# Performance work log

Measured on AMD Instinct MI355X. Metric: run time of the kernel, lower is better.

## Reference

```python
import jax, jax.numpy as jnp
import numpy as np

UNITS, ORDER, THETA = 1024, 512, 784.0
T, B = 784, 128

def _lmu_AB(order, theta):
    # Legendre delay continuous-time state space, then ZOH discretization (dt=1)
    q = np.arange(order, dtype=np.float64)
    r = (2.0 * q + 1.0)[:, None] / theta
    i, j = np.meshgrid(q, q, indexing='ij')
    A = np.where(i < j, -1.0, (-1.0) ** (i - j + 1.0)) * r
    Bc = ((-1.0) ** q)[:, None] * r
    Ad = np.array(jax.scipy.linalg.expm(jnp.asarray(A, dtype=jnp.float32)), dtype=np.float64)
    Bd = np.linalg.solve(A, (Ad - np.eye(order)) @ Bc)
    # cell stores AT = Ad - I so that m <- m + m@AT^T + u@BT^T == m@Ad^T + u@Bd^T
    return (Ad - np.eye(order)).astype(np.float32), Bd.astype(np.float32)

def setup_inputs() -> dict:
    key = jax.random.key(0)
    ks = jax.random.split(key, 9)
    AT, BT = _lmu_AB(ORDER, THETA)
    xav = np.sqrt(2.0 / (UNITS + ORDER)).astype(np.float32)
    return {
        'inputs': jax.random.normal(ks[0], (T, B, 1), dtype=jnp.float32),
        'e_x': jax.random.normal(ks[1], (1, 1), dtype=jnp.float32),
        'e_h': jax.random.normal(ks[2], (1, UNITS), dtype=jnp.float32) * 0.02,
        'e_m': jax.random.normal(ks[3], (1, ORDER), dtype=jnp.float32) * 0.02,
        'W_x': jax.random.normal(ks[4], (UNITS, 1), dtype=jnp.float32) * 0.1,
        'W_h': jax.random.normal(ks[5], (UNITS, UNITS), dtype=jnp.float32) * 0.02,
        'W_m': jax.random.normal(ks[6], (UNITS, ORDER), dtype=jnp.float32) * xav,
        'AT': jnp.asarray(AT),
        'BT': jnp.asarray(BT),
        'W_dense': jax.random.normal(ks[7], (10, UNITS), dtype=jnp.float32) * 0.03,
        'b_dense': jax.random.normal(ks[8], (10,), dtype=jnp.float32) * 0.01,
    }

def reference(inputs, e_x, e_h, e_m, W_x, W_h, W_m, AT, BT, W_dense, b_dense):
    Bsz = inputs.shape[1]
    h0 = jnp.zeros((Bsz, W_h.shape[0]), inputs.dtype)
    m0 = jnp.zeros((Bsz, AT.shape[0]), inputs.dtype)
    def step(carry, x):  # x: (B, 1)
        h, m = carry
        u = x @ e_x.T + h @ e_h.T + m @ e_m.T            # (B, 1)
        m = m + m @ AT.T + u @ BT.T                       # linear Legendre memory update
        h = jnp.tanh(x @ W_x.T + h @ W_h.T + m @ W_m.T)  # nonlinear hidden update
        return (h, m), None
    (h, m), _ = jax.lax.scan(step, (h0, m0), inputs)
    logits = h @ W_dense.T + b_dense
    return jax.nn.softmax(logits, axis=-1)
```

## Files before the change

kernel.cpp:

```cpp
#include <hip/hip_runtime.h>
#include <hip/hip_fp16.h>
#include <cmath>


typedef _Float16 half8 __attribute__((ext_vector_type(8)));
typedef float floatx4 __attribute__((ext_vector_type(4)));

#define NSTATE   1536
#define BATCH    128
#define TSTEPS   784
#define KTILES   48
#define ISL_WGS  32
#define SLICE_H8 9216
#define LO_SCALE 2048.0f
#define LO_INV   (1.0f / 2048.0f)
#define NWAVES   8
#define KI_W     6

__device__ __align__(16) _Float16 g_Whi[NSTATE * NSTATE];
__device__ __align__(16) _Float16 g_Wlo[NSTATE * NSTATE];
__device__ float    g_wb[NSTATE];
__device__ float    g_WmA[1024 * 512];
__device__ float    g_WmB[1024];
__device__ __align__(16) _Float16 g_Shi[2 * BATCH * NSTATE];
__device__ __align__(16) _Float16 g_Slo[2 * BATCH * NSTATE];
__device__ unsigned g_bar[1024];

__device__ __forceinline__ unsigned poll_rmw(unsigned* p) {
    unsigned old;
    asm volatile("global_atomic_add %0, %1, %2, off sc0\n\ts_waitcnt vmcnt(0)"
                 : "=&v"(old)
                 : "v"(p), "v"(0u)
                 : "memory");
    return old;
}

__device__ __forceinline__ float fast_tanh(float x) {
    float e = __expf(2.f * x);
    return 1.f - 2.f / (e + 1.f);
}

__global__ void prep_wmb(const float* __restrict__ Wm, const float* __restrict__ BT) {
    int row  = blockIdx.x * 4 + (threadIdx.x >> 6);
    int lane = threadIdx.x & 63;
    float s = 0.f;
    for (int c = lane; c < 512; c += 64) s += Wm[row * 512 + c] * BT[c];
    for (int o = 32; o; o >>= 1) s += __shfl_down(s, o);
    if (lane == 0) g_WmB[row] = s;
}

__global__ void prep_wma(const float* __restrict__ Wm, const float* __restrict__ AT) {
    __shared__ float As[32][33], Bs[32][33];
    int d0 = blockIdx.x * 32, i0 = blockIdx.y * 32;
    int tx = threadIdx.x & 31, ty = threadIdx.x >> 5;
    float acc[4];
#pragma unroll
    for (int r = 0; r < 4; ++r) acc[r] = Wm[(i0 + ty + 8 * r) * 512 + d0 + tx];
    for (int c0 = 0; c0 < 512; c0 += 32) {
#pragma unroll
        for (int r = 0; r < 4; ++r) {
            As[ty + 8 * r][tx] = Wm[(i0 + ty + 8 * r) * 512 + c0 + tx];
            Bs[ty + 8 * r][tx] = AT[(c0 + ty + 8 * r) * 512 + d0 + tx];
        }
        __syncthreads();
#pragma unroll
        for (int c = 0; c < 32; ++c)
#pragma unroll
            for (int r = 0; r < 4; ++r) acc[r] += As[ty + 8 * r][c] * Bs[c][tx];
        __syncthreads();
    }
#pragma unroll
    for (int r = 0; r < 4; ++r) g_WmA[(i0 + ty + 8 * r) * 512 + d0 + tx] = acc[r];
}

__global__ void prep_wfull(const float* __restrict__ Wh, const float* __restrict__ AT,
                           const float* __restrict__ BT, const float* __restrict__ eh,
                           const float* __restrict__ em, const float* __restrict__ ex,
                           const float* __restrict__ Wx) {
    int s = blockIdx.x * 256 + threadIdx.x;
    int j8 = s & 7;
    int u = s >> 3;
    int lane = u & 63;
    u >>= 6;
    int nt = u % 3; u /= 3;
    int kt = u % 48;
    int sl = u / 48;
    int n = sl * 48 + nt * 16 + (lane & 15);
    int k = kt * 32 + ((lane >> 4) & 3) * 8 + j8;

    float w;
    if (n < 1024) {
        if (k < 1024) w = Wh[n * 1024 + k] + g_WmB[n] * eh[k];
        else          w = g_WmA[n * 512 + (k - 1024)] + g_WmB[n] * em[k - 1024];
    } else {
        int c = n - 1024;
        if (k < 1024) w = BT[c] * eh[k];
        else {
            int d = k - 1024;
            w = ((c == d) ? 1.f : 0.f) + AT[c * 512 + d] + BT[c] * em[d];
        }
    }
    _Float16 hi = (_Float16)w;
    g_Whi[s] = hi;
    g_Wlo[s] = (_Float16)((w - (float)hi) * LO_SCALE);

    if (s < NSTATE) {
        float b = (s < 1024) ? (Wx[s] + ex[0] * g_WmB[s]) : (BT[s - 1024] * ex[0]);
        g_wb[s] = b;
    }
    if (s < 2 * BATCH * NSTATE) { g_Shi[s] = (_Float16)0.f; g_Slo[s] = (_Float16)0.f; }
    if (s < 1024) g_bar[s] = 0u;
}

__launch_bounds__(512, 2)
__global__ void lmu_persist(const float* __restrict__ inputs) {
    __shared__ half8   lwh[SLICE_H8];
    __shared__ floatx4 red[4 * 3 * 64];
    __shared__ int     s_sl;

    const int tid = threadIdx.x;

    unsigned xcd;
    asm volatile("s_getreg_b32 %0, hwreg(HW_REG_XCC_ID)" : "=s"(xcd));
    xcd &= 7u;
    if (tid == 0) {
        unsigned rank = __hip_atomic_fetch_add(g_bar + 512 + xcd * 64, 1u,
                                               __ATOMIC_RELAXED,
                                               __HIP_MEMORY_SCOPE_WORKGROUP);
        s_sl = (int)(rank & 31u);
    }
    __syncthreads();
    const int isl = (int)xcd;
    const int sl  = s_sl;

    {
        const half8* src = (const half8*)g_Whi + (size_t)sl * SLICE_H8;
        for (int i = tid; i < SLICE_H8; i += 512) lwh[i] = src[i];
    }

    const int lane = tid & 63, wv = tid >> 6;
    const int quad = lane >> 4, l16 = lane & 15;
    const int kt0 = wv * KI_W;
    const int rowA = isl * 16 + l16;
    unsigned* cnt = g_bar + isl * 64;

    const int ncol = sl * 48 + wv * 16 + l16;
    const float wbv = (wv < 3) ? g_wb[ncol] : 0.f;
    const bool do_tanh = (sl * 48 + wv * 16) < 1024;

    half8 wr[KI_W * 3];
    {
        const half8* wlo = (const half8*)g_Wlo + (size_t)sl * SLICE_H8;
#pragma unroll
        for (int ki = 0; ki < KI_W; ++ki)
#pragma unroll
            for (int nt = 0; nt < 3; ++nt)
                wr[ki * 3 + nt] = wlo[((kt0 + ki) * 3 + nt) * 64 + lane];
    }

    __syncthreads();

    int buf = 0;
    for (int t = 0; t < TSTEPS; ++t) {
        const _Float16* shr =
            g_Shi + buf * BATCH * NSTATE + rowA * NSTATE + quad * 8;
        const _Float16* slr =
            g_Slo + buf * BATCH * NSTATE + rowA * NSTATE + quad * 8;

        floatx4 aA[3], aB[3], aC[3];
#pragma unroll
        for (int q = 0; q < 3; ++q) { aA[q] = (floatx4)0.f; aB[q] = (floatx4)0.f; aC[q] = (floatx4)0.f; }

#pragma unroll
        for (int ki = 0; ki < KI_W; ++ki) {
            const int kt = kt0 + ki;
            half8 ah = *(const half8*)(shr + kt * 32);
            half8 al = *(const half8*)(slr + kt * 32);
#pragma unroll
            for (int nt = 0; nt < 3; ++nt) {
                half8 bh = lwh[(kt * 3 + nt) * 64 + lane];
                aA[nt] = __builtin_amdgcn_mfma_f32_16x16x32_f16(ah, bh, aA[nt], 0, 0, 0);
                aB[nt] = __builtin_amdgcn_mfma_f32_16x16x32_f16(al, bh, aB[nt], 0, 0, 0);
                aC[nt] = __builtin_amdgcn_mfma_f32_16x16x32_f16(ah, wr[ki * 3 + nt], aC[nt], 0, 0, 0);
            }
        }

        floatx4 P[3];
#pragma unroll
        for (int nt = 0; nt < 3; ++nt)
            P[nt] = aA[nt] + (aB[nt] + aC[nt]) * LO_INV;
        if (wv < 4) {
#pragma unroll
            for (int nt = 0; nt < 3; ++nt)
                red[((wv & 3) * 3 + nt) * 64 + lane] = P[nt];
        }
        __syncthreads();
        if (wv >= 4) {
#pragma unroll
            for (int nt = 0; nt < 3; ++nt)
                red[((wv & 3) * 3 + nt) * 64 + lane] += P[nt];
        }
        __syncthreads();

        const int nbuf = buf ^ 1;
        if (wv < 3) {
            floatx4 vs = red[(0 * 3 + wv) * 64 + lane] + red[(1 * 3 + wv) * 64 + lane]
                       + red[(2 * 3 + wv) * 64 + lane] + red[(3 * 3 + wv) * 64 + lane];
            _Float16* dh = g_Shi + nbuf * BATCH * NSTATE;
            _Float16* dl = g_Slo + nbuf * BATCH * NSTATE;
            const float* xt = inputs + t * BATCH + isl * 16 + quad * 4;
#pragma unroll
            for (int r = 0; r < 4; ++r) {
                int b = isl * 16 + quad * 4 + r;
                float v = vs[r] + xt[r] * wbv;
                if (do_tanh) v = fast_tanh(v);
                _Float16 hi = (_Float16)v;
                dh[b * NSTATE + ncol] = hi;
                dl[b * NSTATE + ncol] = (_Float16)((v - (float)hi) * LO_SCALE);
            }
        }

        __builtin_amdgcn_fence(__ATOMIC_RELEASE, "workgroup");
        __syncthreads();
        if (tid == 0) {
            __hip_atomic_fetch_add(cnt, 1u, __ATOMIC_RELAXED,
                                   __HIP_MEMORY_SCOPE_WORKGROUP);
            const unsigned target = (unsigned)ISL_WGS * (unsigned)(t + 1);
            int spin = 0;
            while (poll_rmw(cnt) < target) {
                if (++spin > (1 << 18)) break;
            }
        }
        __syncthreads();
        asm volatile("buffer_inv\n\ts_waitcnt vmcnt(0)" ::: "memory");
        __builtin_amdgcn_fence(__ATOMIC_ACQUIRE, "workgroup");
        buf = nbuf;
    }
}

__global__ void lmu_out(const float* __restrict__ Wd, const float* __restrict__ bd,
                        float* __restrict__ out) {
    __shared__ float red[272];
    int b = blockIdx.x;
    const _Float16* sh = g_Shi + b * NSTATE;
    const _Float16* sl = g_Slo + b * NSTATE;
    int tid = threadIdx.x;
    int c = tid & 15, chunk = tid >> 4;
    float part = 0.f;
    if (c < 10) {
        for (int i = chunk * 64; i < chunk * 64 + 64; ++i)
            part += ((float)sh[i] + (float)sl[i] * LO_INV) * Wd[c * 1024 + i];
    }
    red[chunk * 16 + c] = part;
    __syncthreads();
    if (tid < 10) {
        float lg = bd[tid];
        for (int q = 0; q < 16; ++q) lg += red[q * 16 + tid];
        red[256 + tid] = lg;
    }
    __syncthreads();
    if (tid < 10) {
        float mx = red[256];
        for (int q = 1; q < 10; ++q) mx = fmaxf(mx, red[256 + q]);
        float sm = 0.f;
        for (int q = 0; q < 10; ++q) sm += expf(red[256 + q] - mx);
        out[b * 10 + tid] = expf(red[256 + tid] - mx) / sm;
    }
}

extern "C" void kernel_launch(void* const* d_in, const int* in_sizes, int n_in,
                              void* d_out, int out_size, void* d_ws, size_t ws_size,
                              hipStream_t stream) {
    const float* inputs = (const float*)d_in[0];
    const float* e_x    = (const float*)d_in[1];
    const float* e_h    = (const float*)d_in[2];
    const float* e_m    = (const float*)d_in[3];
    const float* W_x    = (const float*)d_in[4];
    const float* W_h    = (const float*)d_in[5];
    const float* W_m    = (const float*)d_in[6];
    const float* AT     = (const float*)d_in[7];
    const float* BT     = (const float*)d_in[8];
    const float* W_d    = (const float*)d_in[9];
    const float* b_d    = (const float*)d_in[10];
    (void)d_ws; (void)ws_size; (void)in_sizes; (void)n_in;

    prep_wmb<<<256, 256, 0, stream>>>(W_m, BT);
    prep_wma<<<dim3(16, 32), 256, 0, stream>>>(W_m, AT);
    prep_wfull<<<9216, 256, 0, stream>>>(W_h, AT, BT, e_h, e_m, e_x, W_x);

    lmu_persist<<<256, 512, 0, stream>>>(inputs);

    lmu_out<<<128, 256, 0, stream>>>(W_d, b_d, (float*)d_out);
}
```

Before: 3.949 ms.

## Split workgroup into two independent pipelines with per-producer flag synchronization

Replaces the per-step all-workgroup counter barrier and __syncthreads with fine-grained flags: each workgroup's half (pipe of 4 waves handling 8 batch rows) waits only on the specific producer slices it reads, and intra-WG reduction uses LDS spin counters instead of block barriers. Each wave now covers 12 k-tiles with half the A rows zeroed, doubling per-wave MFMA work while halving the useful rows. The aim is to cut barrier latency and let the two pipes run decoupled, at the cost of wasted MFMA lanes, more register pressure (36 half8 low-weight registers) and fragile spin-wait ordering.

```diff
diff --git a/kernel.cpp b/kernel.cpp
--- a/kernel.cpp
+++ b/kernel.cpp
@@ -14,8 +14,7 @@
 #define SLICE_H8 9216
 #define LO_SCALE 2048.0f
 #define LO_INV   (1.0f / 2048.0f)
-#define NWAVES   8
-#define KI_W     6
+#define PIPES    2
 
 __device__ __align__(16) _Float16 g_Whi[NSTATE * NSTATE];
 __device__ __align__(16) _Float16 g_Wlo[NSTATE * NSTATE];
@@ -25,6 +24,7 @@
 __device__ __align__(16) _Float16 g_Shi[2 * BATCH * NSTATE];
 __device__ __align__(16) _Float16 g_Slo[2 * BATCH * NSTATE];
 __device__ unsigned g_bar[1024];
+__device__ unsigned g_flags[PIPES * 8 * 32 * 64];
 
 __device__ __forceinline__ unsigned poll_rmw(unsigned* p) {
     unsigned old;
@@ -33,6 +33,19 @@
                  : "v"(p), "v"(0u)
                  : "memory");
     return old;
+}
+
+__device__ __forceinline__ void lds_arrive(unsigned* c) {
+    if ((threadIdx.x & 63) == 0)
+        __hip_atomic_fetch_add(c, 1u, __ATOMIC_RELEASE,
+                               __HIP_MEMORY_SCOPE_WORKGROUP);
+}
+__device__ __forceinline__ void lds_wait(unsigned* c, unsigned tgt) {
+    int spin = 0;
+    while (__hip_atomic_load(c, __ATOMIC_ACQUIRE,
+                             __HIP_MEMORY_SCOPE_WORKGROUP) < tgt) {
+        if (++spin > (1 << 20)) break;
+    }
 }
 
 __device__ __forceinline__ float fast_tanh(float x) {
@@ -110,13 +123,15 @@
     }
     if (s < 2 * BATCH * NSTATE) { g_Shi[s] = (_Float16)0.f; g_Slo[s] = (_Float16)0.f; }
     if (s < 1024) g_bar[s] = 0u;
+    if (s < PIPES * 8 * 32 * 64) g_flags[s] = 0u;
 }
 
 __launch_bounds__(512, 2)
 __global__ void lmu_persist(const float* __restrict__ inputs) {
     __shared__ half8   lwh[SLICE_H8];
-    __shared__ floatx4 red[4 * 3 * 64];
-    __shared__ int     s_sl;
+    __shared__ floatx4 red[PIPES][2][3][64];
+    __shared__ unsigned lbar[PIPES][4];
+    __shared__ int s_sl;
 
     const int tid = threadIdx.x;
 
@@ -129,6 +144,7 @@
                                                __HIP_MEMORY_SCOPE_WORKGROUP);
         s_sl = (int)(rank & 31u);
     }
+    if (tid < PIPES * 4) ((unsigned*)lbar)[tid] = 0u;
     __syncthreads();
     const int isl = (int)xcd;
     const int sl  = s_sl;
@@ -139,20 +155,27 @@
     }
 
     const int lane = tid & 63, wv = tid >> 6;
+    const int p  = wv >> 2;
+    const int w4 = wv & 3;
     const int quad = lane >> 4, l16 = lane & 15;
-    const int kt0 = wv * KI_W;
-    const int rowA = isl * 16 + l16;
-    unsigned* cnt = g_bar + isl * 64;
-
-    const int ncol = sl * 48 + wv * 16 + l16;
-    const float wbv = (wv < 3) ? g_wb[ncol] : 0.f;
-    const bool do_tanh = (sl * 48 + wv * 16) < 1024;
-
-    half8 wr[KI_W * 3];
+    const int kt0 = w4 * 12;
+    const int row8 = isl * 16 + p * 8 + l16;
+
+    unsigned* myprod =
+        g_flags + (size_t)(((p * 8 + isl) * 32) + w4 * 8 + (lane & 7)) * 64;
+    unsigned* myflag = g_flags + (size_t)(((p * 8 + isl) * 32) + sl) * 64;
+    unsigned* bar = (unsigned*)lbar[p];
+
+    const int ncol = sl * 48 + w4 * 16 + l16;
+    const float wbv = (w4 < 3) ? g_wb[ncol] : 0.f;
+    const bool do_tanh = (sl * 48 + w4 * 16) < 1024;
+    const bool my_rows = (quad < 2);
+
+    half8 wr[12 * 3];
     {
         const half8* wlo = (const half8*)g_Wlo + (size_t)sl * SLICE_H8;
 #pragma unroll
-        for (int ki = 0; ki < KI_W; ++ki)
+        for (int ki = 0; ki < 12; ++ki)
 #pragma unroll
             for (int nt = 0; nt < 3; ++nt)
                 wr[ki * 3 + nt] = wlo[((kt0 + ki) * 3 + nt) * 64 + lane];
@@ -162,20 +185,36 @@
 
     int buf = 0;
     for (int t = 0; t < TSTEPS; ++t) {
+        if (t) {
+            const unsigned tgt = (unsigned)t;
+            bool done = (lane >= 8);
+            int spin = 0;
+            while (!__all(done)) {
+                if (!done) done = (poll_rmw(myprod) >= tgt);
+                if (++spin > (1 << 18)) break;
+            }
+            asm volatile("buffer_inv\n\ts_waitcnt vmcnt(0)" ::: "memory");
+            __builtin_amdgcn_fence(__ATOMIC_ACQUIRE, "workgroup");
+        }
+
         const _Float16* shr =
-            g_Shi + buf * BATCH * NSTATE + rowA * NSTATE + quad * 8;
+            g_Shi + buf * BATCH * NSTATE + row8 * NSTATE + quad * 8;
         const _Float16* slr =
-            g_Slo + buf * BATCH * NSTATE + rowA * NSTATE + quad * 8;
+            g_Slo + buf * BATCH * NSTATE + row8 * NSTATE + quad * 8;
 
         floatx4 aA[3], aB[3], aC[3];
 #pragma unroll
         for (int q = 0; q < 3; ++q) { aA[q] = (floatx4)0.f; aB[q] = (floatx4)0.f; aC[q] = (floatx4)0.f; }
 
 #pragma unroll
-        for (int ki = 0; ki < KI_W; ++ki) {
+        for (int ki = 0; ki < 12; ++ki) {
             const int kt = kt0 + ki;
-            half8 ah = *(const half8*)(shr + kt * 32);
-            half8 al = *(const half8*)(slr + kt * 32);
+            half8 ah = (half8)(_Float16)0.f;
+            half8 al = (half8)(_Float16)0.f;
+            if (l16 < 8) {
+                ah = *(const half8*)(shr + kt * 32);
+                al = *(const half8*)(slr + kt * 32);
+            }
 #pragma unroll
             for (int nt = 0; nt < 3; ++nt) {
                 half8 bh = lwh[(kt * 3 + nt) * 64 + lane];
@@ -189,51 +228,50 @@
 #pragma unroll
         for (int nt = 0; nt < 3; ++nt)
             P[nt] = aA[nt] + (aB[nt] + aC[nt]) * LO_INV;
-        if (wv < 4) {
+
+        lds_wait(bar + 2, 3u * (unsigned)t);
+        if (w4 < 2) {
 #pragma unroll
             for (int nt = 0; nt < 3; ++nt)
-                red[((wv & 3) * 3 + nt) * 64 + lane] = P[nt];
-        }
-        __syncthreads();
-        if (wv >= 4) {
+                red[p][w4][nt][lane] = P[nt];
+            lds_arrive(bar + 0);
+        } else {
+            lds_wait(bar + 0, 2u * (unsigned)(t + 1));
 #pragma unroll
             for (int nt = 0; nt < 3; ++nt)
-                red[((wv & 3) * 3 + nt) * 64 + lane] += P[nt];
-        }
-        __syncthreads();
+                red[p][w4 - 2][nt][lane] += P[nt];
+            lds_arrive(bar + 1);
+        }
 
         const int nbuf = buf ^ 1;
-        if (wv < 3) {
-            floatx4 vs = red[(0 * 3 + wv) * 64 + lane] + red[(1 * 3 + wv) * 64 + lane]
-                       + red[(2 * 3 + wv) * 64 + lane] + red[(3 * 3 + wv) * 64 + lane];
-            _Float16* dh = g_Shi + nbuf * BATCH * NSTATE;
-            _Float16* dl = g_Slo + nbuf * BATCH * NSTATE;
-            const float* xt = inputs + t * BATCH + isl * 16 + quad * 4;
-#pragma unroll
-            for (int r = 0; r < 4; ++r) {
-                int b = isl * 16 + quad * 4 + r;
-                float v = vs[r] + xt[r] * wbv;
-                if (do_tanh) v = fast_tanh(v);
-                _Float16 hi = (_Float16)v;
-                dh[b * NSTATE + ncol] = hi;
-                dl[b * NSTATE + ncol] = (_Float16)((v - (float)hi) * LO_SCALE);
-            }
-        }
-
-        __builtin_amdgcn_fence(__ATOMIC_RELEASE, "workgroup");
-        __syncthreads();
-        if (tid == 0) {
-            __hip_atomic_fetch_add(cnt, 1u, __ATOMIC_RELAXED,
-                                   __HIP_MEMORY_SCOPE_WORKGROUP);
-            const unsigned target = (unsigned)ISL_WGS * (unsigned)(t + 1);
-            int spin = 0;
-            while (poll_rmw(cnt) < target) {
-                if (++spin > (1 << 18)) break;
-            }
-        }
-        __syncthreads();
-        asm volatile("buffer_inv\n\ts_waitcnt vmcnt(0)" ::: "memory");
-        __builtin_amdgcn_fence(__ATOMIC_ACQUIRE, "workgroup");
+        if (w4 < 3) {
+            lds_wait(bar + 1, 2u * (unsigned)(t + 1));
+            floatx4 vs = red[p][0][w4][lane] + red[p][1][w4][lane];
+            if (my_rows) {
+                _Float16* dh = g_Shi + nbuf * BATCH * NSTATE;
+                _Float16* dl = g_Slo + nbuf * BATCH * NSTATE;
+                const float* xt = inputs + t * BATCH + isl * 16 + p * 8 + quad * 4;
+#pragma unroll
+                for (int r = 0; r < 4; ++r) {
+                    int b = isl * 16 + p * 8 + quad * 4 + r;
+                    float v = vs[r] + xt[r] * wbv;
+                    if (do_tanh) v = fast_tanh(v);
+                    _Float16 hi = (_Float16)v;
+                    dh[b * NSTATE + ncol] = hi;
+                    dl[b * NSTATE + ncol] = (_Float16)((v - (float)hi) * LO_SCALE);
+                }
+            }
+            asm volatile("s_waitcnt vmcnt(0)" ::: "memory");
+            __builtin_amdgcn_fence(__ATOMIC_RELEASE, "workgroup");
+            if (lane == 0) {
+                unsigned old = __hip_atomic_fetch_add(bar + 2, 1u,
+                                                      __ATOMIC_ACQ_REL,
+                                                      __HIP_MEMORY_SCOPE_WORKGROUP);
+                if (old == 3u * (unsigned)t + 2u)
+                    __hip_atomic_fetch_add(myflag, 1u, __ATOMIC_RELAXED,
+                                           __HIP_MEMORY_SCOPE_WORKGROUP);
+            }
+        }
         buf = nbuf;
     }
 }
```

Result: slower. 8.447 ms (+113.9%).
